# Kernel optimization log

Measured on AMD Instinct MI355X. Metric: run time of the kernel, lower is better.

## Reference

```python
import jax, jax.numpy as jnp
import numpy as np

B, S, D, H = 4, 2048, 1024, 16
DQ = D // H  # 64


def setup_inputs() -> dict:
    key = jax.random.key(0)
    ks = jax.random.split(key, 7)
    return {
        "q": jax.random.normal(ks[0], (B, S, D), dtype=jnp.float32),
        "k": jax.random.normal(ks[1], (B, S, D), dtype=jnp.float32),
        "v": jax.random.normal(ks[2], (B, S, D), dtype=jnp.float32),
        "mask": jax.random.randint(ks[3], (B, 1, S, S), 0, 2, dtype=jnp.int32),
        "weight_q": jax.random.normal(ks[4], (H, D, DQ), dtype=jnp.float32),
        "weight_k": jax.random.normal(ks[5], (H, D, DQ), dtype=jnp.float32),
        "weight_v": jax.random.normal(ks[6], (H, D, DQ), dtype=jnp.float32),
    }


def reference(q, k, v, mask, weight_q, weight_k, weight_v):
    # Per-head projections: [b,s,d] x [h,d,q] -> [b,h,s,q]
    Q = jnp.einsum('bsd,hdq->bhsq', q, weight_q)
    K = jnp.einsum('bsd,hdq->bhsq', k, weight_k)
    V = jnp.einsum('bsd,hdq->bhsq', v, weight_v)
    scale = 1.0 / jnp.sqrt(jnp.float32(DQ))
    scores = jnp.einsum('bhsq,bhtq->bhst', Q, K) * scale  # [b,h,s,s]
    scores = jnp.where(mask == 0, jnp.float32(-1e9), scores)
    scores = jax.nn.softmax(scores, axis=-1)
    # Faithful to torch.einsum('bhss,bhsq->bhsq', ...): repeated index 's'
    # takes the DIAGONAL of the attention matrix, scaling V elementwise.
    diag = jnp.diagonal(scores, axis1=2, axis2=3)  # [b,h,s]
    x = diag[..., None] * V  # [b,h,s,dq]
    return x
```

## Files before the change

### kernel.cpp

```cpp
#include <hip/hip_runtime.h>


#define BB 4
#define SS 2048
#define DD 1024
#define HH 16
#define DQQ 64

typedef unsigned short u16;
typedef unsigned int u32;
typedef __attribute__((ext_vector_type(8))) short bf16x8;
typedef __attribute__((ext_vector_type(4))) float f32x4;

static constexpr float SCALE_L2E = 0.125f * 1.44269504f;
static constexpr float NEG9 = -1e9f;

#define MFMA16(a, b, c) __builtin_amdgcn_mfma_f32_16x16x32_bf16((a), (b), (c), 0, 0, 0)

__device__ __forceinline__ float ex2(float x) {
#if __has_builtin(__builtin_amdgcn_exp2f)
    return __builtin_amdgcn_exp2f(x);
#else
    return __expf(x * 0.69314718055994531f);
#endif
}

__device__ __forceinline__ u16 bfrne(float x) {
    u32 u = __float_as_uint(x);
    return (u16)((u + 0x7fffu + ((u >> 16) & 1u)) >> 16);
}
__device__ __forceinline__ u32 pk2(float a, float b) {
    return (u32)bfrne(a) | ((u32)bfrne(b) << 16);
}
__device__ __forceinline__ float lo_f(u32 p) { return __uint_as_float(p << 16); }
__device__ __forceinline__ float hi_f(u32 p) { return __uint_as_float(p & 0xFFFF0000u); }

union U4V { u32 u[4]; bf16x8 v; uint4 q4; };

__global__ __launch_bounds__(256) void mask_pack_k(const int* __restrict__ mask,
                                                   u32* __restrict__ bits) {
    const int w = blockIdx.x * 256 + threadIdx.x;
    const long long row  = (long long)(w >> 6);
    const long long base = row * SS + (long long)((w & 63) << 5);
    const int4* mp = reinterpret_cast<const int4*>(mask + base);
    u32 v = 0;
#pragma unroll
    for (int j = 0; j < 8; ++j) {
        int4 m4 = mp[j];
        v |= (m4.x != 0 ? 1u : 0u) << (4 * j + 0);
        v |= (m4.y != 0 ? 1u : 0u) << (4 * j + 1);
        v |= (m4.z != 0 ? 1u : 0u) << (4 * j + 2);
        v |= (m4.w != 0 ? 1u : 0u) << (4 * j + 3);
    }
    bits[w] = v;
}

__global__ __launch_bounds__(256) void wsplit2_k(const float* __restrict__ W,
                                                 u16* __restrict__ Ph,
                                                 u16* __restrict__ Pl,
                                                 int has_lo, float scale) {
    const int f = blockIdx.x * 4 + (threadIdx.x >> 6);
    const int lane = threadIdx.x & 63;
    const int qtile = f >> 5, kc = f & 31;
    const int h = qtile >> 2, q = ((qtile & 3) << 4) + (lane & 15);
    const int d0 = kc * 32 + (lane >> 4) * 8;
    float x[8];
#pragma unroll
    for (int j = 0; j < 8; ++j)
        x[j] = W[((long long)h * DD + d0 + j) * DQQ + q] * scale;
    U4V hh;
    hh.u[0] = pk2(x[0], x[1]); hh.u[1] = pk2(x[2], x[3]);
    hh.u[2] = pk2(x[4], x[5]); hh.u[3] = pk2(x[6], x[7]);
    const long long base = ((long long)f << 9) + lane * 8;
    *reinterpret_cast<uint4*>(Ph + base) = hh.q4;
    if (has_lo) {
        U4V ll;
        ll.u[0] = pk2(x[0] - lo_f(hh.u[0]), x[1] - hi_f(hh.u[0]));
        ll.u[1] = pk2(x[2] - lo_f(hh.u[1]), x[3] - hi_f(hh.u[1]));
        ll.u[2] = pk2(x[4] - lo_f(hh.u[2]), x[5] - hi_f(hh.u[2]));
        ll.u[3] = pk2(x[6] - lo_f(hh.u[3]), x[7] - hi_f(hh.u[3]));
        *reinterpret_cast<uint4*>(Pl + base) = ll.q4;
    }
}

__global__ __launch_bounds__(256) void splitx_k(const float* __restrict__ X,
                                                u16* __restrict__ Xh,
                                                u16* __restrict__ Xl,
                                                int has_lo) {
    const int g = blockIdx.x * 256 + threadIdx.x;
    const int kc = g & 31;
    const int row = g >> 5;
    const float* xp = X + ((long long)row << 10) + kc * 32;
    const int lrow = row & 15;
    const long long base = (((long long)(row >> 4) * 32 + kc) << 9);
    float4 f[8];
#pragma unroll
    for (int i = 0; i < 8; ++i) f[i] = reinterpret_cast<const float4*>(xp)[i];
#pragma unroll
    for (int lg = 0; lg < 4; ++lg) {
        const float v0 = f[2 * lg].x, v1 = f[2 * lg].y, v2 = f[2 * lg].z, v3 = f[2 * lg].w;
        const float v4 = f[2 * lg + 1].x, v5 = f[2 * lg + 1].y,
                    v6 = f[2 * lg + 1].z, v7 = f[2 * lg + 1].w;
        U4V hh;
        hh.u[0] = pk2(v0, v1); hh.u[1] = pk2(v2, v3);
        hh.u[2] = pk2(v4, v5); hh.u[3] = pk2(v6, v7);
        const long long o = base + (lrow + 16 * lg) * 8;
        *reinterpret_cast<uint4*>(Xh + o) = hh.q4;
        if (has_lo) {
            U4V ll;
            ll.u[0] = pk2(v0 - lo_f(hh.u[0]), v1 - hi_f(hh.u[0]));
            ll.u[1] = pk2(v2 - lo_f(hh.u[1]), v3 - hi_f(hh.u[1]));
            ll.u[2] = pk2(v4 - lo_f(hh.u[2]), v5 - hi_f(hh.u[2]));
            ll.u[3] = pk2(v6 - lo_f(hh.u[3]), v7 - hi_f(hh.u[3]));
            *reinterpret_cast<uint4*>(Xl + o) = ll.q4;
        }
    }
}

__global__ __launch_bounds__(256) void proj_qk2_k(
        const u16* __restrict__ Xh, const u16* __restrict__ Xl,
        const u16* __restrict__ Wph, const u16* __restrict__ Wpl,
        u16* __restrict__ Oh, u16* __restrict__ Ol) {
    const int t = threadIdx.x, lane = t & 63, wid = t >> 6;
    const int lrow = lane & 15, lgrp = lane >> 4;
    const int qt0 = blockIdx.y * 8 + (wid >> 1) * 4;
    const int st0 = blockIdx.x * 8 + (wid & 1) * 4;

    f32x4 acc[4][4];
#pragma unroll
    for (int i = 0; i < 4; ++i)
#pragma unroll
        for (int j = 0; j < 4; ++j) acc[i][j] = (f32x4){0.f, 0.f, 0.f, 0.f};

#pragma unroll 2
    for (int kc = 0; kc < 32; ++kc) {
        bf16x8 Ah[4], Al[4], Bh[4], Bl[4];
#pragma unroll
        for (int mt = 0; mt < 4; ++mt) {
            const long long ab = (((long long)(qt0 + mt) * 32 + kc) << 9) + lane * 8;
            Ah[mt] = *reinterpret_cast<const bf16x8*>(Wph + ab);
            Al[mt] = *reinterpret_cast<const bf16x8*>(Wpl + ab);
        }
#pragma unroll
        for (int nt = 0; nt < 4; ++nt) {
            const long long bb = (((long long)(st0 + nt) * 32 + kc) << 9) + lane * 8;
            Bh[nt] = *reinterpret_cast<const bf16x8*>(Xh + bb);
            Bl[nt] = *reinterpret_cast<const bf16x8*>(Xl + bb);
        }
#pragma unroll
        for (int mt = 0; mt < 4; ++mt)
#pragma unroll
            for (int nt = 0; nt < 4; ++nt) {
                acc[mt][nt] = MFMA16(Ah[mt], Bh[nt], acc[mt][nt]);
                acc[mt][nt] = MFMA16(Ah[mt], Bl[nt], acc[mt][nt]);
                acc[mt][nt] = MFMA16(Al[mt], Bh[nt], acc[mt][nt]);
            }
    }

#pragma unroll
    for (int mt = 0; mt < 4; ++mt) {
        const int qtg = qt0 + mt;
        const int hh_ = qtg >> 2;
        const int qb = ((qtg & 3) << 4) + (lgrp << 2);
#pragma unroll
        for (int nt = 0; nt < 4; ++nt) {
            const int c = (st0 + nt) * 16 + lrow;
            const int b = c >> 11, s = c & 2047;
            const int bh = (b << 4) + hh_;
            const float x0 = acc[mt][nt][0], x1 = acc[mt][nt][1],
                        x2 = acc[mt][nt][2], x3 = acc[mt][nt][3];
            const u32 h01 = pk2(x0, x1), h23 = pk2(x2, x3);
            const u32 l01 = pk2(x0 - lo_f(h01), x1 - hi_f(h01));
            const u32 l23 = pk2(x2 - lo_f(h23), x3 - hi_f(h23));
            const int st = s >> 4, kcq = qb >> 5;
            const int lanep = lrow + (((qb & 31) >> 3) << 4);
            const long long oi = ((((long long)bh * 128 + st) * 2 + kcq) << 9)
                                 + lanep * 8 + (qb & 7);
            *reinterpret_cast<uint2*>(Oh + oi) = make_uint2(h01, h23);
            *reinterpret_cast<uint2*>(Ol + oi) = make_uint2(l01, l23);
        }
    }
}

__global__ __launch_bounds__(256) void proj_v2_k(
        const u16* __restrict__ Xh, const u16* __restrict__ Wph,
        u16* __restrict__ Vb) {
    const int t = threadIdx.x, lane = t & 63, wid = t >> 6;
    const int lrow = lane & 15, lgrp = lane >> 4;
    const int qt0 = blockIdx.y * 8 + (wid >> 1) * 4;
    const int st0 = blockIdx.x * 8 + (wid & 1) * 4;

    f32x4 acc[4][4];
#pragma unroll
    for (int i = 0; i < 4; ++i)
#pragma unroll
        for (int j = 0; j < 4; ++j) acc[i][j] = (f32x4){0.f, 0.f, 0.f, 0.f};

#pragma unroll 2
    for (int kc = 0; kc < 32; ++kc) {
        bf16x8 Ah[4], Bh[4];
#pragma unroll
        for (int mt = 0; mt < 4; ++mt) {
            const long long ab = (((long long)(qt0 + mt) * 32 + kc) << 9) + lane * 8;
            Ah[mt] = *reinterpret_cast<const bf16x8*>(Wph + ab);
        }
#pragma unroll
        for (int nt = 0; nt < 4; ++nt) {
            const long long bb = (((long long)(st0 + nt) * 32 + kc) << 9) + lane * 8;
            Bh[nt] = *reinterpret_cast<const bf16x8*>(Xh + bb);
        }
#pragma unroll
        for (int mt = 0; mt < 4; ++mt)
#pragma unroll
            for (int nt = 0; nt < 4; ++nt)
                acc[mt][nt] = MFMA16(Ah[mt], Bh[nt], acc[mt][nt]);
    }

#pragma unroll
    for (int mt = 0; mt < 4; ++mt) {
        const int qtg = qt0 + mt;
        const int hh_ = qtg >> 2;
        const int qb = ((qtg & 3) << 4) + (lgrp << 2);
#pragma unroll
        for (int nt = 0; nt < 4; ++nt) {
            const int c = (st0 + nt) * 16 + lrow;
            const int b = c >> 11, s = c & 2047;
            const int bh = (b << 4) + hh_;
            const u32 h01 = pk2(acc[mt][nt][0], acc[mt][nt][1]);
            const u32 h23 = pk2(acc[mt][nt][2], acc[mt][nt][3]);
            const long long oi = ((long long)bh * SS + s) * DQQ + qb;
            *reinterpret_cast<uint2*>(Vb + oi) = make_uint2(h01, h23);
        }
    }
}

__global__ __launch_bounds__(256) void attn_k(
        const u16* __restrict__ Qh, const u16* __restrict__ Ql,
        const u16* __restrict__ Kh, const u16* __restrict__ Kl,
        const u16* __restrict__ Vb, const u32* __restrict__ bits,
        float* __restrict__ out) {
    const int qt = blockIdx.x, h = blockIdx.y, b = blockIdx.z;
    const int s0 = qt * 128;
    const long long bh = b * HH + h;
    const int t = threadIdx.x, lane = t & 63, wid = t >> 6;
    const int l15 = lane & 15, lgrp = lane >> 4;

    __shared__ u16 Kst[2][2][4096];
    __shared__ float sdiag[128];
    __shared__ float dwgt[128];

    bf16x8 qfh[2][2], qfl[2][2];
#pragma unroll
    for (int mt = 0; mt < 2; ++mt)
#pragma unroll
        for (int ks = 0; ks < 2; ++ks) {
            const int stq = qt * 8 + wid * 2 + mt;
            const long long gi = (((bh * 128 + stq) * 2 + ks) << 9) + lane * 8;
            qfh[mt][ks] = *reinterpret_cast<const bf16x8*>(&Qh[gi]);
            qfl[mt][ks] = *reinterpret_cast<const bf16x8*>(&Ql[gi]);
        }

    const u32 kbase = (u32)(bh * 131072u) + (u32)t * 8u;
    bf16x8 sh[2], sl[2];
    auto loadK = [&](int cchN) {
        const u32 o = kbase + (u32)cchN * 4096u;
        sh[0] = *reinterpret_cast<const bf16x8*>(Kh + o);
        sl[0] = *reinterpret_cast<const bf16x8*>(Kl + o);
        sh[1] = *reinterpret_cast<const bf16x8*>(Kh + o + 2048u);
        sl[1] = *reinterpret_cast<const bf16x8*>(Kl + o + 2048u);
    };
    auto stageK = [&](int buf) {
#pragma unroll
        for (int i = 0; i < 2; ++i) {
            *reinterpret_cast<bf16x8*>(&Kst[buf][0][(t + i * 256) * 8]) = sh[i];
            *reinterpret_cast<bf16x8*>(&Kst[buf][1][(t + i * 256) * 8]) = sl[i];
        }
    };

    const u32* __restrict__ brow = bits + (((long long)b * SS + s0) << 6);
    u32 moff[2][4];
#pragma unroll
    for (int mt = 0; mt < 2; ++mt)
#pragma unroll
        for (int r = 0; r < 4; ++r)
            moff[mt][r] = (u32)((wid * 32 + mt * 16 + lgrp * 4 + r) << 6);

    const f32x4 zz = (f32x4){0.f, 0.f, 0.f, 0.f};

    loadK(2 * qt);     stageK(0);
    loadK(2 * qt + 1); stageK(1);
    __syncthreads();
    {
        const int bufA = wid >> 1;
        const int nt0 = (wid & 1) * 2;
        const int cA = 2 * qt + bufA;
#pragma unroll
        for (int mt = 0; mt < 2; ++mt) {
            const int ntd = nt0 + mt;
            bf16x8 kh0 = *reinterpret_cast<const bf16x8*>(&Kst[bufA][0][(ntd * 2 + 0) * 512 + lane * 8]);
            bf16x8 kh1 = *reinterpret_cast<const bf16x8*>(&Kst[bufA][0][(ntd * 2 + 1) * 512 + lane * 8]);
            bf16x8 kl0 = *reinterpret_cast<const bf16x8*>(&Kst[bufA][1][(ntd * 2 + 0) * 512 + lane * 8]);
            bf16x8 kl1 = *reinterpret_cast<const bf16x8*>(&Kst[bufA][1][(ntd * 2 + 1) * 512 + lane * 8]);
            f32x4 a = MFMA16(qfh[mt][0], kh0, zz);
            a = MFMA16(qfh[mt][1], kh1, a);
            a = MFMA16(qfh[mt][0], kl0, a);
            a = MFMA16(qfh[mt][1], kl1, a);
            a = MFMA16(qfl[mt][0], kh0, a);
            a = MFMA16(qfl[mt][1], kh1, a);
#pragma unroll
            for (int r = 0; r < 4; ++r) {
                if (l15 == lgrp * 4 + r) {
                    const u32 word = brow[moff[mt][r] + (u32)(cA * 2) + (u32)(ntd >> 1)];
                    const u32 bit = (word >> ((ntd & 1) * 16 + l15)) & 1u;
                    sdiag[wid * 32 + mt * 16 + lgrp * 4 + r] = bit ? a[r] : NEG9;
                }
            }
        }
    }
    __syncthreads();

    float sdA[2][4], nsd[2][4];
#pragma unroll
    for (int mt = 0; mt < 2; ++mt) {
        float4 v4 = *reinterpret_cast<const float4*>(&sdiag[wid * 32 + mt * 16 + lgrp * 4]);
        sdA[mt][0] = v4.x; sdA[mt][1] = v4.y; sdA[mt][2] = v4.z; sdA[mt][3] = v4.w;
#pragma unroll
        for (int r = 0; r < 4; ++r) nsd[mt][r] = NEG9 - sdA[mt][r];
    }

    loadK(0); stageK(0);
    float srun[2][4];
#pragma unroll
    for (int mt = 0; mt < 2; ++mt)
#pragma unroll
        for (int r = 0; r < 4; ++r) srun[mt][r] = 0.f;

    for (int cch = 0; cch < 32; ++cch) {
        const int cur = cch & 1;
        __syncthreads();
        if (cch + 1 < 32) loadK(cch + 1);

        uint2 mw[2][4];
        const u32 c2 = (u32)(cch * 2);
#pragma unroll
        for (int mt = 0; mt < 2; ++mt)
#pragma unroll
            for (int r = 0; r < 4; ++r)
                mw[mt][r] = *reinterpret_cast<const uint2*>(brow + moff[mt][r] + c2);

        bf16x8 kfh[4][2], kfl[4][2];
#pragma unroll
        for (int nt = 0; nt < 4; ++nt)
#pragma unroll
            for (int ks = 0; ks < 2; ++ks) {
                kfh[nt][ks] = *reinterpret_cast<const bf16x8*>(&Kst[cur][0][(nt * 2 + ks) * 512 + lane * 8]);
                kfl[nt][ks] = *reinterpret_cast<const bf16x8*>(&Kst[cur][1][(nt * 2 + ks) * 512 + lane * 8]);
            }

        f32x4 sc[2][4];
#pragma unroll
        for (int mt = 0; mt < 2; ++mt)
#pragma unroll
            for (int nt = 0; nt < 4; ++nt) {
                f32x4 a = MFMA16(qfh[mt][0], kfh[nt][0], zz);
                a = MFMA16(qfh[mt][1], kfh[nt][1], a);
                a = MFMA16(qfh[mt][0], kfl[nt][0], a);
                a = MFMA16(qfh[mt][1], kfl[nt][1], a);
                a = MFMA16(qfl[mt][0], kfh[nt][0], a);
                a = MFMA16(qfl[mt][1], kfh[nt][1], a);
                sc[mt][nt] = a;
            }

#pragma unroll
        for (int mt = 0; mt < 2; ++mt)
#pragma unroll
            for (int r = 0; r < 4; ++r) {
                const u32 w0s = mw[mt][r].x >> l15;
                const u32 w1s = mw[mt][r].y >> l15;
                const float sd = sdA[mt][r], nd = nsd[mt][r];
                float d0 = sc[mt][0][r] - sd;
                float d1 = sc[mt][1][r] - sd;
                float d2 = sc[mt][2][r] - sd;
                float d3 = sc[mt][3][r] - sd;
                d0 = (w0s & 1u)       ? d0 : nd;
                d1 = (w0s & 0x10000u) ? d1 : nd;
                d2 = (w1s & 1u)       ? d2 : nd;
                d3 = (w1s & 0x10000u) ? d3 : nd;
                srun[mt][r] += (ex2(d0) + ex2(d1)) + (ex2(d2) + ex2(d3));
            }

        if (cch + 1 < 32) stageK(cur ^ 1);
    }

#pragma unroll
    for (int mt = 0; mt < 2; ++mt)
#pragma unroll
        for (int r = 0; r < 4; ++r) {
            float so = srun[mt][r];
#pragma unroll
            for (int st = 1; st < 16; st <<= 1)
                so += __shfl_xor(so, st, 64);
            if (l15 == 0)
                dwgt[wid * 32 + mt * 16 + lgrp * 4 + r] = 1.0f / so;
        }
    __syncthreads();

    const int orow = t >> 1, oc = (t & 1) * 32;
    const float w = dwgt[orow];
    const u16* vp = Vb + (bh * SS + s0 + orow) * DQQ + oc;
    float* op = out + (bh * SS + s0 + orow) * DQQ + oc;
#pragma unroll
    for (int j = 0; j < 8; ++j) {
        u32 pv = *reinterpret_cast<const u32*>(&vp[j * 4 + 0]);
        u32 pv2 = *reinterpret_cast<const u32*>(&vp[j * 4 + 2]);
        float4 o;
        o.x = lo_f(pv) * w;  o.y = hi_f(pv) * w;
        o.z = lo_f(pv2) * w; o.w = hi_f(pv2) * w;
        reinterpret_cast<float4*>(op)[j] = o;
    }
}

extern "C" void kernel_launch(void* const* d_in, const int* in_sizes, int n_in,
                              void* d_out, int out_size, void* d_ws, size_t ws_size,
                              hipStream_t stream) {
    (void)in_sizes; (void)n_in; (void)out_size; (void)ws_size;
    const float* q    = (const float*)d_in[0];
    const float* k    = (const float*)d_in[1];
    const float* v    = (const float*)d_in[2];
    const int*   mask = (const int*)d_in[3];
    const float* wq   = (const float*)d_in[4];
    const float* wk   = (const float*)d_in[5];
    const float* wv   = (const float*)d_in[6];

    const size_t NP2 = (size_t)BB * HH * SS * DQQ * 2;
    char* wsp = (char*)d_ws;
    u16* Qh = (u16*)wsp;            wsp += NP2;
    u16* Ql = (u16*)wsp;            wsp += NP2;
    u16* Kh = (u16*)wsp;            wsp += NP2;
    u16* Kl = (u16*)wsp;            wsp += NP2;
    u16* Vb = (u16*)wsp;            wsp += NP2;
    u16* Wph = (u16*)wsp;           wsp += (size_t)3 * 2048 * 512 * 2;
    u16* Wpl = (u16*)wsp;           wsp += (size_t)2 * 2048 * 512 * 2;
    u32* bits = (u32*)wsp;          wsp += (size_t)BB * SS * 64 * 4;
    u16* extra = (u16*)wsp;

    u16* Xh_q = Kh;    u16* Xl_q = Kl;
    u16* Xh_k = Vb;    u16* Xl_k = extra;
    u16* Xh_v = extra;

    mask_pack_k<<<dim3(2048), dim3(256), 0, stream>>>(mask, bits);
    wsplit2_k<<<dim3(512), dim3(256), 0, stream>>>(wq, Wph, Wpl, 1, SCALE_L2E);
    wsplit2_k<<<dim3(512), dim3(256), 0, stream>>>(wk, Wph + (1 << 20), Wpl + (1 << 20), 1, 1.0f);
    wsplit2_k<<<dim3(512), dim3(256), 0, stream>>>(wv, Wph + (2u << 20), Wph, 0, 1.0f);

    splitx_k<<<dim3(1024), dim3(256), 0, stream>>>(q, Xh_q, Xl_q, 1);
    proj_qk2_k<<<dim3(64, 8), dim3(256), 0, stream>>>(Xh_q, Xl_q, Wph, Wpl, Qh, Ql);

    splitx_k<<<dim3(1024), dim3(256), 0, stream>>>(k, Xh_k, Xl_k, 1);
    proj_qk2_k<<<dim3(64, 8), dim3(256), 0, stream>>>(Xh_k, Xl_k,
                                                      Wph + (1 << 20), Wpl + (1 << 20),
                                                      Kh, Kl);

    splitx_k<<<dim3(1024), dim3(256), 0, stream>>>(v, Xh_v, Xh_v, 0);
    proj_v2_k<<<dim3(64, 8), dim3(256), 0, stream>>>(Xh_v, Wph + (2u << 20), Vb);

    attn_k<<<dim3(16, 16, 4), dim3(256), 0, stream>>>(Qh, Ql, Kh, Kl, Vb, bits,
                                                      (float*)d_out);
}
```

Baseline: 335.7 us.

## Load K fragments directly from global, remap grid for L2 locality, fold diag subtraction into MFMA

The attention kernel stops staging K tiles through shared memory with double buffering and __syncthreads. Each wave now reads its K fragments straight from global memory and relies on L2/MALL reuse. The grid is flattened and remapped so that the 8 consecutive blocks share a query tile across 8 (b,h) pairs, which is meant to help cache locality and scheduling. The subtraction of the diagonal score is folded into the MFMA accumulator's initial value, which removes per-element subtractions. The trade-off is that each of the four waves fetches the same K data redundantly from global/L2 instead of sharing it from LDS, in exchange for no barriers and higher possible occupancy.

```diff
diff --git a/kernel.cpp b/kernel.cpp
--- a/kernel.cpp
+++ b/kernel.cpp
@@ -239,13 +239,14 @@
         const u16* __restrict__ Kh, const u16* __restrict__ Kl,
         const u16* __restrict__ Vb, const u32* __restrict__ bits,
         float* __restrict__ out) {
-    const int qt = blockIdx.x, h = blockIdx.y, b = blockIdx.z;
+    const int id = blockIdx.x;
+    const int c8 = id & 7, qt = (id >> 3) & 15, g = id >> 7;
+    const int bh = (g << 3) | c8;
+    const int b = bh >> 4;
     const int s0 = qt * 128;
-    const long long bh = b * HH + h;
     const int t = threadIdx.x, lane = t & 63, wid = t >> 6;
     const int l15 = lane & 15, lgrp = lane >> 4;
 
-    __shared__ u16 Kst[2][2][4096];
     __shared__ float sdiag[128];
     __shared__ float dwgt[128];
 
@@ -255,27 +256,12 @@
 #pragma unroll
         for (int ks = 0; ks < 2; ++ks) {
             const int stq = qt * 8 + wid * 2 + mt;
-            const long long gi = (((bh * 128 + stq) * 2 + ks) << 9) + lane * 8;
+            const long long gi = ((((long long)bh * 128 + stq) * 2 + ks) << 9) + lane * 8;
             qfh[mt][ks] = *reinterpret_cast<const bf16x8*>(&Qh[gi]);
             qfl[mt][ks] = *reinterpret_cast<const bf16x8*>(&Ql[gi]);
         }
 
-    const u32 kbase = (u32)(bh * 131072u) + (u32)t * 8u;
-    bf16x8 sh[2], sl[2];
-    auto loadK = [&](int cchN) {
-        const u32 o = kbase + (u32)cchN * 4096u;
-        sh[0] = *reinterpret_cast<const bf16x8*>(Kh + o);
-        sl[0] = *reinterpret_cast<const bf16x8*>(Kl + o);
-        sh[1] = *reinterpret_cast<const bf16x8*>(Kh + o + 2048u);
-        sl[1] = *reinterpret_cast<const bf16x8*>(Kl + o + 2048u);
-    };
-    auto stageK = [&](int buf) {
-#pragma unroll
-        for (int i = 0; i < 2; ++i) {
-            *reinterpret_cast<bf16x8*>(&Kst[buf][0][(t + i * 256) * 8]) = sh[i];
-            *reinterpret_cast<bf16x8*>(&Kst[buf][1][(t + i * 256) * 8]) = sl[i];
-        }
-    };
+    const u32 kfb = (u32)bh * 131072u + (u32)lane * 8u;
 
     const u32* __restrict__ brow = bits + (((long long)b * SS + s0) << 6);
     u32 moff[2][4];
@@ -287,20 +273,17 @@
 
     const f32x4 zz = (f32x4){0.f, 0.f, 0.f, 0.f};
 
-    loadK(2 * qt);     stageK(0);
-    loadK(2 * qt + 1); stageK(1);
-    __syncthreads();
     {
-        const int bufA = wid >> 1;
+        const int cA = 2 * qt + (wid >> 1);
         const int nt0 = (wid & 1) * 2;
-        const int cA = 2 * qt + bufA;
 #pragma unroll
         for (int mt = 0; mt < 2; ++mt) {
             const int ntd = nt0 + mt;
-            bf16x8 kh0 = *reinterpret_cast<const bf16x8*>(&Kst[bufA][0][(ntd * 2 + 0) * 512 + lane * 8]);
-            bf16x8 kh1 = *reinterpret_cast<const bf16x8*>(&Kst[bufA][0][(ntd * 2 + 1) * 512 + lane * 8]);
-            bf16x8 kl0 = *reinterpret_cast<const bf16x8*>(&Kst[bufA][1][(ntd * 2 + 0) * 512 + lane * 8]);
-            bf16x8 kl1 = *reinterpret_cast<const bf16x8*>(&Kst[bufA][1][(ntd * 2 + 1) * 512 + lane * 8]);
+            const u32 o = kfb + (u32)cA * 4096u + (u32)(ntd * 2) * 512u;
+            bf16x8 kh0 = *reinterpret_cast<const bf16x8*>(Kh + o);
+            bf16x8 kh1 = *reinterpret_cast<const bf16x8*>(Kh + o + 512u);
+            bf16x8 kl0 = *reinterpret_cast<const bf16x8*>(Kl + o);
+            bf16x8 kl1 = *reinterpret_cast<const bf16x8*>(Kl + o + 512u);
             f32x4 a = MFMA16(qfh[mt][0], kh0, zz);
             a = MFMA16(qfh[mt][1], kh1, a);
             a = MFMA16(qfh[mt][0], kl0, a);
@@ -320,15 +303,18 @@
     __syncthreads();
 
     float sdA[2][4], nsd[2][4];
+    f32x4 msd[2];
 #pragma unroll
     for (int mt = 0; mt < 2; ++mt) {
         float4 v4 = *reinterpret_cast<const float4*>(&sdiag[wid * 32 + mt * 16 + lgrp * 4]);
         sdA[mt][0] = v4.x; sdA[mt][1] = v4.y; sdA[mt][2] = v4.z; sdA[mt][3] = v4.w;
 #pragma unroll
-        for (int r = 0; r < 4; ++r) nsd[mt][r] = NEG9 - sdA[mt][r];
-    }
-
-    loadK(0); stageK(0);
+        for (int r = 0; r < 4; ++r) {
+            nsd[mt][r] = NEG9 - sdA[mt][r];
+            msd[mt][r] = -sdA[mt][r];
+        }
+    }
+
     float srun[2][4];
 #pragma unroll
     for (int mt = 0; mt < 2; ++mt)
@@ -336,9 +322,7 @@
         for (int r = 0; r < 4; ++r) srun[mt][r] = 0.f;
 
     for (int cch = 0; cch < 32; ++cch) {
-        const int cur = cch & 1;
-        __syncthreads();
-        if (cch + 1 < 32) loadK(cch + 1);
+        const u32 ko = kfb + (u32)cch * 4096u;
 
         uint2 mw[2][4];
         const u32 c2 = (u32)(cch * 2);
@@ -353,8 +337,9 @@
         for (int nt = 0; nt < 4; ++nt)
 #pragma unroll
             for (int ks = 0; ks < 2; ++ks) {
-                kfh[nt][ks] = *reinterpret_cast<const bf16x8*>(&Kst[cur][0][(nt * 2 + ks) * 512 + lane * 8]);
-                kfl[nt][ks] = *reinterpret_cast<const bf16x8*>(&Kst[cur][1][(nt * 2 + ks) * 512 + lane * 8]);
+                const u32 o = ko + (u32)(nt * 2 + ks) * 512u;
+                kfh[nt][ks] = *reinterpret_cast<const bf16x8*>(Kh + o);
+                kfl[nt][ks] = *reinterpret_cast<const bf16x8*>(Kl + o);
             }
 
         f32x4 sc[2][4];
@@ -362,7 +347,7 @@
         for (int mt = 0; mt < 2; ++mt)
 #pragma unroll
             for (int nt = 0; nt < 4; ++nt) {
-                f32x4 a = MFMA16(qfh[mt][0], kfh[nt][0], zz);
+                f32x4 a = MFMA16(qfh[mt][0], kfh[nt][0], msd[mt]);
                 a = MFMA16(qfh[mt][1], kfh[nt][1], a);
                 a = MFMA16(qfh[mt][0], kfl[nt][0], a);
                 a = MFMA16(qfh[mt][1], kfl[nt][1], a);
@@ -377,19 +362,13 @@
             for (int r = 0; r < 4; ++r) {
                 const u32 w0s = mw[mt][r].x >> l15;
                 const u32 w1s = mw[mt][r].y >> l15;
-                const float sd = sdA[mt][r], nd = nsd[mt][r];
-                float d0 = sc[mt][0][r] - sd;
-                float d1 = sc[mt][1][r] - sd;
-                float d2 = sc[mt][2][r] - sd;
-                float d3 = sc[mt][3][r] - sd;
-                d0 = (w0s & 1u)       ? d0 : nd;
-                d1 = (w0s & 0x10000u) ? d1 : nd;
-                d2 = (w1s & 1u)       ? d2 : nd;
-                d3 = (w1s & 0x10000u) ? d3 : nd;
+                const float nd = nsd[mt][r];
+                float d0 = (w0s & 1u)       ? sc[mt][0][r] : nd;
+                float d1 = (w0s & 0x10000u) ? sc[mt][1][r] : nd;
+                float d2 = (w1s & 1u)       ? sc[mt][2][r] : nd;
+                float d3 = (w1s & 0x10000u) ? sc[mt][3][r] : nd;
                 srun[mt][r] += (ex2(d0) + ex2(d1)) + (ex2(d2) + ex2(d3));
             }
-
-        if (cch + 1 < 32) stageK(cur ^ 1);
     }
 
 #pragma unroll
@@ -407,8 +386,8 @@
 
     const int orow = t >> 1, oc = (t & 1) * 32;
     const float w = dwgt[orow];
-    const u16* vp = Vb + (bh * SS + s0 + orow) * DQQ + oc;
-    float* op = out + (bh * SS + s0 + orow) * DQQ + oc;
+    const u16* vp = Vb + (((long long)bh * SS) + s0 + orow) * DQQ + oc;
+    float* op = out + (((long long)bh * SS) + s0 + orow) * DQQ + oc;
 #pragma unroll
     for (int j = 0; j < 8; ++j) {
         u32 pv = *reinterpret_cast<const u32*>(&vp[j * 4 + 0]);
@@ -464,6 +443,6 @@
     splitx_k<<<dim3(1024), dim3(256), 0, stream>>>(v, Xh_v, Xh_v, 0);
     proj_v2_k<<<dim3(64, 8), dim3(256), 0, stream>>>(Xh_v, Wph + (2u << 20), Vb);
 
-    attn_k<<<dim3(16, 16, 4), dim3(256), 0, stream>>>(Qh, Ql, Kh, Kl, Vb, bits,
-                                                      (float*)d_out);
-}
+    attn_k<<<dim3(1024), dim3(256), 0, stream>>>(Qh, Ql, Kh, Kl, Vb, bits,
+                                                 (float*)d_out);
+}
```

New measurement: 350.2 us. 4.3% more time.

## Fuse input bf16 split into projection GEMMs with LDS staging and merge Q/K launches

Applied to the files above, without the earlier changes.

The separate splitx kernels are removed. The projection kernels now read fp32 inputs directly, split them into hi/lo bf16 on the fly, and stage them in double-buffered LDS shared by all warps. Q and K projections are merged into one launch via blockIdx.z, and each warp now computes 8x4 tiles. This is meant to remove the intermediate bf16 round-trip through global memory and cut launch count. The attention kernel also folds the diagonal subtraction into the MFMA accumulator init. The risks are higher register pressure from the 32 accumulators and far fewer blocks (512 and 256) per projection launch.

```diff
diff --git a/kernel.cpp b/kernel.cpp
--- a/kernel.cpp
+++ b/kernel.cpp
@@ -83,98 +83,98 @@
     }
 }
 
-__global__ __launch_bounds__(256) void splitx_k(const float* __restrict__ X,
-                                                u16* __restrict__ Xh,
-                                                u16* __restrict__ Xl,
-                                                int has_lo) {
-    const int g = blockIdx.x * 256 + threadIdx.x;
-    const int kc = g & 31;
-    const int row = g >> 5;
-    const float* xp = X + ((long long)row << 10) + kc * 32;
-    const int lrow = row & 15;
-    const long long base = (((long long)(row >> 4) * 32 + kc) << 9);
-    float4 f[8];
-#pragma unroll
-    for (int i = 0; i < 8; ++i) f[i] = reinterpret_cast<const float4*>(xp)[i];
-#pragma unroll
-    for (int lg = 0; lg < 4; ++lg) {
-        const float v0 = f[2 * lg].x, v1 = f[2 * lg].y, v2 = f[2 * lg].z, v3 = f[2 * lg].w;
-        const float v4 = f[2 * lg + 1].x, v5 = f[2 * lg + 1].y,
-                    v6 = f[2 * lg + 1].z, v7 = f[2 * lg + 1].w;
-        U4V hh;
-        hh.u[0] = pk2(v0, v1); hh.u[1] = pk2(v2, v3);
-        hh.u[2] = pk2(v4, v5); hh.u[3] = pk2(v6, v7);
-        const long long o = base + (lrow + 16 * lg) * 8;
-        *reinterpret_cast<uint4*>(Xh + o) = hh.q4;
-        if (has_lo) {
-            U4V ll;
-            ll.u[0] = pk2(v0 - lo_f(hh.u[0]), v1 - hi_f(hh.u[0]));
-            ll.u[1] = pk2(v2 - lo_f(hh.u[1]), v3 - hi_f(hh.u[1]));
-            ll.u[2] = pk2(v4 - lo_f(hh.u[2]), v5 - hi_f(hh.u[2]));
-            ll.u[3] = pk2(v6 - lo_f(hh.u[3]), v7 - hi_f(hh.u[3]));
-            *reinterpret_cast<uint4*>(Xl + o) = ll.q4;
-        }
-    }
-}
-
-__global__ __launch_bounds__(256) void proj_qk2_k(
-        const u16* __restrict__ Xh, const u16* __restrict__ Xl,
-        const u16* __restrict__ Wph, const u16* __restrict__ Wpl,
-        u16* __restrict__ Oh, u16* __restrict__ Ol) {
+__global__ __launch_bounds__(256) void proj_qk3_k(
+        const float* __restrict__ q_in, const float* __restrict__ k_in,
+        const u16* __restrict__ Wph_all, const u16* __restrict__ Wpl_all,
+        u16* __restrict__ Qh, u16* __restrict__ Ql,
+        u16* __restrict__ Kh, u16* __restrict__ Kl) {
+    const int nb = blockIdx.x, ch = blockIdx.y, z = blockIdx.z;
+    const float* __restrict__ X = z ? k_in : q_in;
+    const u16* __restrict__ Wph = Wph_all + ((long long)z << 20);
+    const u16* __restrict__ Wpl = Wpl_all + ((long long)z << 20);
+    u16* __restrict__ Oh = z ? Kh : Qh;
+    u16* __restrict__ Ol = z ? Kl : Ql;
+
     const int t = threadIdx.x, lane = t & 63, wid = t >> 6;
     const int lrow = lane & 15, lgrp = lane >> 4;
-    const int qt0 = blockIdx.y * 8 + (wid >> 1) * 4;
-    const int st0 = blockIdx.x * 8 + (wid & 1) * 4;
-
-    f32x4 acc[4][4];
-#pragma unroll
-    for (int i = 0; i < 4; ++i)
-#pragma unroll
-        for (int j = 0; j < 4; ++j) acc[i][j] = (f32x4){0.f, 0.f, 0.f, 0.f};
-
-#pragma unroll 2
+
+    __shared__ u16 XhL[2][2048];
+    __shared__ u16 XlL[2][2048];
+
+    const int srow = t >> 2, sg = t & 3;
+    const float* xrow = X + ((long long)(nb * 64 + srow) << 10) + sg * 8;
+    const int soff = (srow >> 4) * 512 + ((srow & 15) + 16 * sg) * 8;
+
+    float4 xf0, xf1;
+    auto loadX = [&](int kc) {
+        xf0 = reinterpret_cast<const float4*>(xrow + kc * 32)[0];
+        xf1 = reinterpret_cast<const float4*>(xrow + kc * 32)[1];
+    };
+    auto stageX = [&](int buf) {
+        U4V hh, ll;
+        hh.u[0] = pk2(xf0.x, xf0.y); hh.u[1] = pk2(xf0.z, xf0.w);
+        hh.u[2] = pk2(xf1.x, xf1.y); hh.u[3] = pk2(xf1.z, xf1.w);
+        ll.u[0] = pk2(xf0.x - lo_f(hh.u[0]), xf0.y - hi_f(hh.u[0]));
+        ll.u[1] = pk2(xf0.z - lo_f(hh.u[1]), xf0.w - hi_f(hh.u[1]));
+        ll.u[2] = pk2(xf1.x - lo_f(hh.u[2]), xf1.y - hi_f(hh.u[2]));
+        ll.u[3] = pk2(xf1.z - lo_f(hh.u[3]), xf1.w - hi_f(hh.u[3]));
+        *reinterpret_cast<uint4*>(&XhL[buf][soff]) = hh.q4;
+        *reinterpret_cast<uint4*>(&XlL[buf][soff]) = ll.q4;
+    };
+
+    f32x4 acc[8][4];
+#pragma unroll
+    for (int i = 0; i < 8; ++i)
+#pragma unroll
+        for (int st = 0; st < 4; ++st) acc[i][st] = (f32x4){0.f, 0.f, 0.f, 0.f};
+
+    const int qtb = ch * 32 + wid * 8;
+
+    loadX(0); stageX(0);
     for (int kc = 0; kc < 32; ++kc) {
-        bf16x8 Ah[4], Al[4], Bh[4], Bl[4];
-#pragma unroll
-        for (int mt = 0; mt < 4; ++mt) {
-            const long long ab = (((long long)(qt0 + mt) * 32 + kc) << 9) + lane * 8;
-            Ah[mt] = *reinterpret_cast<const bf16x8*>(Wph + ab);
-            Al[mt] = *reinterpret_cast<const bf16x8*>(Wpl + ab);
-        }
-#pragma unroll
-        for (int nt = 0; nt < 4; ++nt) {
-            const long long bb = (((long long)(st0 + nt) * 32 + kc) << 9) + lane * 8;
-            Bh[nt] = *reinterpret_cast<const bf16x8*>(Xh + bb);
-            Bl[nt] = *reinterpret_cast<const bf16x8*>(Xl + bb);
-        }
-#pragma unroll
-        for (int mt = 0; mt < 4; ++mt)
-#pragma unroll
-            for (int nt = 0; nt < 4; ++nt) {
-                acc[mt][nt] = MFMA16(Ah[mt], Bh[nt], acc[mt][nt]);
-                acc[mt][nt] = MFMA16(Ah[mt], Bl[nt], acc[mt][nt]);
-                acc[mt][nt] = MFMA16(Al[mt], Bh[nt], acc[mt][nt]);
+        const int cur = kc & 1;
+        __syncthreads();
+        if (kc + 1 < 32) loadX(kc + 1);
+
+        bf16x8 Bh[4], Bl[4];
+#pragma unroll
+        for (int st = 0; st < 4; ++st) {
+            Bh[st] = *reinterpret_cast<const bf16x8*>(&XhL[cur][st * 512 + lane * 8]);
+            Bl[st] = *reinterpret_cast<const bf16x8*>(&XlL[cur][st * 512 + lane * 8]);
+        }
+#pragma unroll
+        for (int i = 0; i < 8; ++i) {
+            const long long ab = (((long long)(qtb + i) * 32 + kc) << 9) + lane * 8;
+            bf16x8 Ah = *reinterpret_cast<const bf16x8*>(Wph + ab);
+            bf16x8 Al = *reinterpret_cast<const bf16x8*>(Wpl + ab);
+#pragma unroll
+            for (int st = 0; st < 4; ++st) {
+                acc[i][st] = MFMA16(Ah, Bh[st], acc[i][st]);
+                acc[i][st] = MFMA16(Ah, Bl[st], acc[i][st]);
+                acc[i][st] = MFMA16(Al, Bh[st], acc[i][st]);
             }
-    }
-
-#pragma unroll
-    for (int mt = 0; mt < 4; ++mt) {
-        const int qtg = qt0 + mt;
+        }
+        if (kc + 1 < 32) stageX(cur ^ 1);
+    }
+
+#pragma unroll
+    for (int i = 0; i < 8; ++i) {
+        const int qtg = qtb + i;
         const int hh_ = qtg >> 2;
         const int qb = ((qtg & 3) << 4) + (lgrp << 2);
 #pragma unroll
-        for (int nt = 0; nt < 4; ++nt) {
-            const int c = (st0 + nt) * 16 + lrow;
+        for (int st = 0; st < 4; ++st) {
+            const int c = (nb * 4 + st) * 16 + lrow;
             const int b = c >> 11, s = c & 2047;
             const int bh = (b << 4) + hh_;
-            const float x0 = acc[mt][nt][0], x1 = acc[mt][nt][1],
-                        x2 = acc[mt][nt][2], x3 = acc[mt][nt][3];
+            const float x0 = acc[i][st][0], x1 = acc[i][st][1],
+                        x2 = acc[i][st][2], x3 = acc[i][st][3];
             const u32 h01 = pk2(x0, x1), h23 = pk2(x2, x3);
             const u32 l01 = pk2(x0 - lo_f(h01), x1 - hi_f(h01));
             const u32 l23 = pk2(x2 - lo_f(h23), x3 - hi_f(h23));
-            const int st = s >> 4, kcq = qb >> 5;
+            const int stq = s >> 4, kcq = qb >> 5;
             const int lanep = lrow + (((qb & 31) >> 3) << 4);
-            const long long oi = ((((long long)bh * 128 + st) * 2 + kcq) << 9)
+            const long long oi = ((((long long)bh * 128 + stq) * 2 + kcq) << 9)
                                  + lanep * 8 + (qb & 7);
             *reinterpret_cast<uint2*>(Oh + oi) = make_uint2(h01, h23);
             *reinterpret_cast<uint2*>(Ol + oi) = make_uint2(l01, l23);
@@ -182,52 +182,72 @@
     }
 }
 
-__global__ __launch_bounds__(256) void proj_v2_k(
-        const u16* __restrict__ Xh, const u16* __restrict__ Wph,
+__global__ __launch_bounds__(256) void proj_v3_k(
+        const float* __restrict__ v_in, const u16* __restrict__ Wph,
         u16* __restrict__ Vb) {
+    const int nb = blockIdx.x, ch = blockIdx.y;
     const int t = threadIdx.x, lane = t & 63, wid = t >> 6;
     const int lrow = lane & 15, lgrp = lane >> 4;
-    const int qt0 = blockIdx.y * 8 + (wid >> 1) * 4;
-    const int st0 = blockIdx.x * 8 + (wid & 1) * 4;
-
-    f32x4 acc[4][4];
-#pragma unroll
-    for (int i = 0; i < 4; ++i)
-#pragma unroll
-        for (int j = 0; j < 4; ++j) acc[i][j] = (f32x4){0.f, 0.f, 0.f, 0.f};
-
-#pragma unroll 2
+
+    __shared__ u16 XhL[2][2048];
+
+    const int srow = t >> 2, sg = t & 3;
+    const float* xrow = v_in + ((long long)(nb * 64 + srow) << 10) + sg * 8;
+    const int soff = (srow >> 4) * 512 + ((srow & 15) + 16 * sg) * 8;
+
+    float4 xf0, xf1;
+    auto loadX = [&](int kc) {
+        xf0 = reinterpret_cast<const float4*>(xrow + kc * 32)[0];
+        xf1 = reinterpret_cast<const float4*>(xrow + kc * 32)[1];
+    };
+    auto stageX = [&](int buf) {
+        U4V hh;
+        hh.u[0] = pk2(xf0.x, xf0.y); hh.u[1] = pk2(xf0.z, xf0.w);
+        hh.u[2] = pk2(xf1.x, xf1.y); hh.u[3] = pk2(xf1.z, xf1.w);
+        *reinterpret_cast<uint4*>(&XhL[buf][soff]) = hh.q4;
+    };
+
+    f32x4 acc[8][4];
+#pragma unroll
+    for (int i = 0; i < 8; ++i)
+#pragma unroll
+        for (int st = 0; st < 4; ++st) acc[i][st] = (f32x4){0.f, 0.f, 0.f, 0.f};
+
+    const int qtb = ch * 32 + wid * 8;
+
+    loadX(0); stageX(0);
     for (int kc = 0; kc < 32; ++kc) {
-        bf16x8 Ah[4], Bh[4];
-#pragma unroll
-        for (int mt = 0; mt < 4; ++mt) {
-            const long long ab = (((long long)(qt0 + mt) * 32 + kc) << 9) + lane * 8;
-            Ah[mt] = *reinterpret_cast<const bf16x8*>(Wph + ab);
-        }
-#pragma unroll
-        for (int nt = 0; nt < 4; ++nt) {
-            const long long bb = (((long long)(st0 + nt) * 32 + kc) << 9) + lane * 8;
-            Bh[nt] = *reinterpret_cast<const bf16x8*>(Xh + bb);
-        }
-#pragma unroll
-        for (int mt = 0; mt < 4; ++mt)
-#pragma unroll
-            for (int nt = 0; nt < 4; ++nt)
-                acc[mt][nt] = MFMA16(Ah[mt], Bh[nt], acc[mt][nt]);
-    }
-
-#pragma unroll
-    for (int mt = 0; mt < 4; ++mt) {
-        const int qtg = qt0 + mt;
+        const int cur = kc & 1;
+        __syncthreads();
+        if (kc + 1 < 32) loadX(kc + 1);
+
+        bf16x8 Bh[4];
+#pragma unroll
+        for (int st = 0; st < 4; ++st)
+            Bh[st] = *reinterpret_cast<const bf16x8*>(&XhL[cur][st * 512 + lane * 8]);
+#pragma unroll
+        for (int i = 0; i < 8; ++i) {
+            const long long ab = (((long long)(qtb + i) * 32 + kc) << 9) + lane * 8;
+            bf16x8 Ah = *reinterpret_cast<const bf16x8*>(Wph + ab);
+#pragma unroll
+            for (int st = 0; st < 4; ++st)
+                acc[i][st] = MFMA16(Ah, Bh[st], acc[i][st]);
+        }
+        if (kc + 1 < 32) stageX(cur ^ 1);
+    }
+
+#pragma unroll
+    for (int i = 0; i < 8; ++i) {
+        const int qtg = qtb + i;
         const int hh_ = qtg >> 2;
         const int qb = ((qtg & 3) << 4) + (lgrp << 2);
 #pragma unroll
-        for (int nt = 0; nt < 4; ++nt) {
-            const int c = (st0 + nt) * 16 + lrow;
+        for (int st = 0; st < 4; ++st) {
+            const int c = (nb * 4 + st) * 16 + lrow;
             const int b = c >> 11, s = c & 2047;
             const int bh = (b << 4) + hh_;
-            const u32 h01 = pk2(acc[mt][nt][0], acc[mt][nt][1]);
-            const u32 h23 = pk2(acc[mt][nt][2], acc[mt][nt][3]);
+            const u32 h01 = pk2(acc[i][st][0], acc[i][st][1]);
+            const u32 h23 = pk2(acc[i][st][2], acc[i][st][3]);
             const long long oi = ((long long)bh * SS + s) * DQQ + qb;
             *reinterpret_cast<uint2*>(Vb + oi) = make_uint2(h01, h23);
         }
@@ -320,12 +340,16 @@
     __syncthreads();
 
     float sdA[2][4], nsd[2][4];
+    f32x4 msd[2];
 #pragma unroll
     for (int mt = 0; mt < 2; ++mt) {
         float4 v4 = *reinterpret_cast<const float4*>(&sdiag[wid * 32 + mt * 16 + lgrp * 4]);
         sdA[mt][0] = v4.x; sdA[mt][1] = v4.y; sdA[mt][2] = v4.z; sdA[mt][3] = v4.w;
 #pragma unroll
-        for (int r = 0; r < 4; ++r) nsd[mt][r] = NEG9 - sdA[mt][r];
+        for (int r = 0; r < 4; ++r) {
+            nsd[mt][r] = NEG9 - sdA[mt][r];
+            msd[mt][r] = -sdA[mt][r];
+        }
     }
 
     loadK(0); stageK(0);
@@ -362,7 +386,7 @@
         for (int mt = 0; mt < 2; ++mt)
 #pragma unroll
             for (int nt = 0; nt < 4; ++nt) {
-                f32x4 a = MFMA16(qfh[mt][0], kfh[nt][0], zz);
+                f32x4 a = MFMA16(qfh[mt][0], kfh[nt][0], msd[mt]);
                 a = MFMA16(qfh[mt][1], kfh[nt][1], a);
                 a = MFMA16(qfh[mt][0], kfl[nt][0], a);
                 a = MFMA16(qfh[mt][1], kfl[nt][1], a);
@@ -377,15 +401,11 @@
             for (int r = 0; r < 4; ++r) {
                 const u32 w0s = mw[mt][r].x >> l15;
                 const u32 w1s = mw[mt][r].y >> l15;
-                const float sd = sdA[mt][r], nd = nsd[mt][r];
-                float d0 = sc[mt][0][r] - sd;
-                float d1 = sc[mt][1][r] - sd;
-                float d2 = sc[mt][2][r] - sd;
-                float d3 = sc[mt][3][r] - sd;
-                d0 = (w0s & 1u)       ? d0 : nd;
-                d1 = (w0s & 0x10000u) ? d1 : nd;
-                d2 = (w1s & 1u)       ? d2 : nd;
-                d3 = (w1s & 0x10000u) ? d3 : nd;
+                const float nd = nsd[mt][r];
+                float d0 = (w0s & 1u)       ? sc[mt][0][r] : nd;
+                float d1 = (w0s & 0x10000u) ? sc[mt][1][r] : nd;
+                float d2 = (w1s & 1u)       ? sc[mt][2][r] : nd;
+                float d3 = (w1s & 0x10000u) ? sc[mt][3][r] : nd;
                 srun[mt][r] += (ex2(d0) + ex2(d1)) + (ex2(d2) + ex2(d3));
             }
 
@@ -441,28 +461,16 @@
     u16* Vb = (u16*)wsp;            wsp += NP2;
     u16* Wph = (u16*)wsp;           wsp += (size_t)3 * 2048 * 512 * 2;
     u16* Wpl = (u16*)wsp;           wsp += (size_t)2 * 2048 * 512 * 2;
-    u32* bits = (u32*)wsp;          wsp += (size_t)BB * SS * 64 * 4;
-    u16* extra = (u16*)wsp;
-
-    u16* Xh_q = Kh;    u16* Xl_q = Kl;
-    u16* Xh_k = Vb;    u16* Xl_k = extra;
-    u16* Xh_v = extra;
+    u32* bits = (u32*)wsp;
 
     mask_pack_k<<<dim3(2048), dim3(256), 0, stream>>>(mask, bits);
     wsplit2_k<<<dim3(512), dim3(256), 0, stream>>>(wq, Wph, Wpl, 1, SCALE_L2E);
     wsplit2_k<<<dim3(512), dim3(256), 0, stream>>>(wk, Wph + (1 << 20), Wpl + (1 << 20), 1, 1.0f);
     wsplit2_k<<<dim3(512), dim3(256), 0, stream>>>(wv, Wph + (2u << 20), Wph, 0, 1.0f);
 
-    splitx_k<<<dim3(1024), dim3(256), 0, stream>>>(q, Xh_q, Xl_q, 1);
-    proj_qk2_k<<<dim3(64, 8), dim3(256), 0, stream>>>(Xh_q, Xl_q, Wph, Wpl, Qh, Ql);
-
-    splitx_k<<<dim3(1024), dim3(256), 0, stream>>>(k, Xh_k, Xl_k, 1);
-    proj_qk2_k<<<dim3(64, 8), dim3(256), 0, stream>>>(Xh_k, Xl_k,
-                                                      Wph + (1 << 20), Wpl + (1 << 20),
-                                                      Kh, Kl);
-
-    splitx_k<<<dim3(1024), dim3(256), 0, stream>>>(v, Xh_v, Xh_v, 0);
-    proj_v2_k<<<dim3(64, 8), dim3(256), 0, stream>>>(Xh_v, Wph + (2u << 20), Vb);
+    proj_qk3_k<<<dim3(128, 2, 2), dim3(256), 0, stream>>>(q, k, Wph, Wpl,
+                                                          Qh, Ql, Kh, Kl);
+    proj_v3_k<<<dim3(128, 2), dim3(256), 0, stream>>>(v, Wph + (2u << 20), Vb);
 
     attn_k<<<dim3(16, 16, 4), dim3(256), 0, stream>>>(Qh, Ql, Kh, Kl, Vb, bits,
                                                       (float*)d_out);
```

After: 356.2 us. 6.1% more time.
